# Kernel tuning notes

Hardware: AMD Instinct MI355X
Metric: run time of the kernel (lower is better)

## Reference

```python
import math
import jax, jax.numpy as jnp
import numpy as np

N, T, C = 4, 2048, 1024
H, DQK, DH = 16, 64, 4096
DV = C // H  # 64
EPS = 1e-5


def new_gelu(x):
    c = math.sqrt(2.0 / math.pi)
    return 0.5 * x * (1.0 + jnp.tanh(c * (x + 0.044715 * x ** 3)))


def layer_norm(x, w, b):
    mu = jnp.mean(x, axis=-1, keepdims=True)
    var = jnp.mean(jnp.square(x - mu), axis=-1, keepdims=True)
    return (x - mu) * jax.lax.rsqrt(var + EPS) * w + b


def setup_inputs() -> dict:
    key = jax.random.key(0)
    ks = jax.random.split(key, 8)
    def randw(k, *d):
        return jax.random.normal(k, d, dtype=jnp.float32) / math.sqrt(d[-1])
    x = jax.random.normal(ks[0], (N, T, C), dtype=jnp.float32)
    return {
        "x": x,
        "ln1_w": jnp.ones((C,), jnp.float32),
        "ln1_b": jnp.zeros((C,), jnp.float32),
        "w_q": randw(ks[1], H, DQK, C),
        "w_k": randw(ks[2], H, DQK, C),
        "w_v": randw(ks[3], H, DV, C),
        "ln2_w": jnp.ones((C,), jnp.float32),
        "ln2_b": jnp.zeros((C,), jnp.float32),
        "fc1_w": randw(ks[4], DH, C),
        "fc1_b": jnp.zeros((DH,), jnp.float32),
        "fc2_w": randw(ks[5], C, DH),
        "fc2_b": jnp.zeros((C,), jnp.float32),
    }


def attention(x, w_q, w_k, w_v):
    q = jnp.einsum('ntc,hdc->nhtd', x, w_q)
    k = jnp.einsum('ntc,hdc->nhtd', x, w_k)
    v = jnp.einsum('ntc,hdc->nhtd', x, w_v)
    a = jnp.einsum('nhtd,nhsd->nhts', q, k) / math.sqrt(DQK)
    t = jnp.arange(x.shape[1])
    causal = t[None, None, :, None] < t[None, None, None, :]  # mask future
    a = jnp.where(causal, -jnp.inf, a)
    a = jax.nn.softmax(a, axis=3)
    y = jnp.einsum('nhts,nhsd->nthd', a, v)
    return y.reshape(y.shape[0], y.shape[1], -1)


def reference(x, ln1_w, ln1_b, w_q, w_k, w_v, ln2_w, ln2_b, fc1_w, fc1_b, fc2_w, fc2_b):
    x = x + attention(layer_norm(x, ln1_w, ln1_b), w_q, w_k, w_v)
    h = layer_norm(x, ln2_w, ln2_b)
    h = new_gelu(h @ fc1_w.T + fc1_b) @ fc2_w.T + fc2_b
    return x + h
```

## Files before the change

kernel.cpp:

```cpp
#include <hip/hip_runtime.h>
#include <stdint.h>

typedef __bf16 bf16;
typedef __bf16 bf16x8 __attribute__((ext_vector_type(8)));
typedef __bf16 bf16x4 __attribute__((ext_vector_type(4)));
typedef float  f32x4  __attribute__((ext_vector_type(4)));

#define AS1 __attribute__((address_space(1)))
#define AS3 __attribute__((address_space(3)))

__device__ __forceinline__ void gload16(void* l, const void* g) {
  __builtin_amdgcn_global_load_lds((AS1 void*)(g), (AS3 void*)(l), 16, 0, 0);
}

#define NB 4
#define TT 2048
#define CC 1024
#define HH 16
#define DD 64
#define DHID 4096
#define MM (NB*TT)

__global__ __launch_bounds__(256)
void cvt_kernel(const float* __restrict__ wq, const float* __restrict__ wk,
                const float* __restrict__ wvv, const float* __restrict__ f1,
                const float* __restrict__ f2, bf16* __restrict__ dst) {
  const int NCH = 2883584;
  for (int ch = blockIdx.x*256 + threadIdx.x; ch < NCH; ch += gridDim.x*256) {
    const float* s; int base;
    if (ch < 262144)       { s = wq;  base = 0; }
    else if (ch < 524288)  { s = wk;  base = 262144; }
    else if (ch < 786432)  { s = wvv; base = 524288; }
    else if (ch < 1835008) { s = f1;  base = 786432; }
    else                   { s = f2;  base = 1835008; }
    float4 v = ((const float4*)s)[ch - base];
    bf16x4 o = { (bf16)v.x, (bf16)v.y, (bf16)v.z, (bf16)v.w };
    *(bf16x4*)(dst + (size_t)ch*4) = o;
  }
}

__global__ __launch_bounds__(256)
void ln_kernel(const float* __restrict__ x, const float* __restrict__ w,
               const float* __restrict__ b, bf16* __restrict__ out) {
  const int row = blockIdx.x;
  const int t = threadIdx.x;
  const float4 v = ((const float4*)(x + (size_t)row*CC))[t];
  float s  = v.x + v.y + v.z + v.w;
  float sq = v.x*v.x + v.y*v.y + v.z*v.z + v.w*v.w;
  #pragma unroll
  for (int m = 1; m < 64; m <<= 1) {
    s  += __shfl_xor(s, m, 64);
    sq += __shfl_xor(sq, m, 64);
  }
  __shared__ float red[8];
  const int wv = t >> 6;
  if ((t & 63) == 0) { red[wv] = s; red[4+wv] = sq; }
  __syncthreads();
  s  = red[0]+red[1]+red[2]+red[3];
  sq = red[4]+red[5]+red[6]+red[7];
  const float mu = s * (1.0f/CC);
  const float rs = rsqrtf(sq*(1.0f/CC) - mu*mu + 1e-5f);
  const float4 wv4 = ((const float4*)w)[t];
  const float4 bv4 = ((const float4*)b)[t];
  bf16x4 o = { (bf16)((v.x-mu)*rs*wv4.x + bv4.x),
               (bf16)((v.y-mu)*rs*wv4.y + bv4.y),
               (bf16)((v.z-mu)*rs*wv4.z + bv4.z),
               (bf16)((v.w-mu)*rs*wv4.w + bv4.w) };
  *(bf16x4*)(out + (size_t)row*CC + t*4) = o;
}

__device__ __forceinline__ float gelu_f(float x) {
  const float kC = 0.7978845608028654f;
  float z = kC * (x + 0.044715f * x*x*x);
  float e = __expf(2.0f*z);
  float th = 1.0f - 2.0f/(e + 1.0f);
  return 0.5f * x * (1.0f + th);
}

template<int MODE>
__global__ __launch_bounds__(256)
void gemm_kernel(const bf16* __restrict__ A, const bf16* __restrict__ B, int K,
                 void* outp, const float* __restrict__ bias, const float* resid) {
  __shared__ __align__(16) bf16 Ab[2][128*32];
  __shared__ __align__(16) bf16 Bb[2][128*32];
  const int tid  = threadIdx.x;
  const int lane = tid & 63;
  const int wv   = tid >> 6;
  const int g = lane >> 4, c = lane & 15;
  const int bm0 = blockIdx.x * 128;
  const int bn0 = blockIdx.y * 128;
  const int wm = (wv >> 1) * 64, wn = (wv & 1) * 64;

  f32x4 acc[4][4] = {};

  const int r0 = tid >> 2, c8 = tid & 3;
  const bf16* a0 = A + (size_t)(bm0 + r0)     * K + c8*8;
  const bf16* a1 = A + (size_t)(bm0 + r0 + 64)* K + c8*8;
  const bf16* b0 = B + (size_t)(bn0 + r0)     * K + c8*8;
  const bf16* b1 = B + (size_t)(bn0 + r0 + 64)* K + c8*8;

  #define GSTAGE(buf, kk)                                   \
    do {                                                    \
      gload16(&Ab[buf][wv*512],     a0 + (kk));             \
      gload16(&Ab[buf][(4+wv)*512], a1 + (kk));             \
      gload16(&Bb[buf][wv*512],     b0 + (kk));             \
      gload16(&Bb[buf][(4+wv)*512], b1 + (kk));             \
    } while (0)

  GSTAGE(0, 0);
  asm volatile("s_waitcnt vmcnt(0)" ::: "memory");
  __syncthreads();

  int cur = 0;
  for (int kt = 0; kt < K; kt += 32) {
    if (kt + 32 < K) GSTAGE(cur ^ 1, kt + 32);
    bf16x8 af[4], bfv[4];
    #pragma unroll
    for (int ms = 0; ms < 4; ++ms)
      af[ms] = *(const bf16x8*)&Ab[cur][(wm + ms*16 + c)*32 + g*8];
    #pragma unroll
    for (int ns = 0; ns < 4; ++ns)
      bfv[ns] = *(const bf16x8*)&Bb[cur][(wn + ns*16 + c)*32 + g*8];
    #pragma unroll
    for (int ms = 0; ms < 4; ++ms) {
      #pragma unroll
      for (int ns = 0; ns < 4; ++ns)
        acc[ms][ns] = __builtin_amdgcn_mfma_f32_16x16x32_bf16(af[ms], bfv[ns], acc[ms][ns], 0, 0, 0);
    }
    asm volatile("s_waitcnt vmcnt(0)" ::: "memory");
    __syncthreads();
    cur ^= 1;
  }

  #pragma unroll
  for (int ms = 0; ms < 4; ++ms) {
    const int m = bm0 + wm + ms*16 + g*4;
    #pragma unroll
    for (int ns = 0; ns < 4; ++ns) {
      const int j = bn0 + wn + ns*16 + c;
      if constexpr (MODE == 0) {
        const int which = j >> 10, hd = j & 1023;
        const int n_ = m >> 11, t_ = m & 2047;
        bf16* dst = (bf16*)outp + (size_t)which*(MM*CC)
                    + (((size_t)(n_*HH + (hd>>6))*TT + t_) << 6) + (hd & 63);
        #pragma unroll
        for (int jj = 0; jj < 4; ++jj)
          dst[(size_t)jj << 6] = (bf16)acc[ms][ns][jj];
      } else if constexpr (MODE == 1) {
        const float bb = bias[j];
        bf16* o = (bf16*)outp;
        #pragma unroll
        for (int jj = 0; jj < 4; ++jj)
          o[(size_t)(m+jj)*DHID + j] = (bf16)gelu_f(acc[ms][ns][jj] + bb);
      } else {
        const float bb = bias[j];
        float* o = (float*)outp;
        #pragma unroll
        for (int jj = 0; jj < 4; ++jj) {
          const size_t ix = (size_t)(m+jj)*CC + j;
          o[ix] = acc[ms][ns][jj] + bb + resid[ix];
        }
      }
    }
  }
  #undef GSTAGE
}

__global__ __launch_bounds__(256)
void attn_kernel(const bf16* __restrict__ qkv, const float* __restrict__ x,
                 float* __restrict__ out) {
  __shared__ __align__(16) bf16 Kb[2][64*64];
  __shared__ __align__(16) bf16 Vt[2][64*64];
  __shared__ __align__(16) bf16 Pb[4][32*64];
  const int tid = threadIdx.x, lane = tid & 63, wv = tid >> 6;
  const int g = lane >> 4, c = lane & 15;
  const int nh = blockIdx.x >> 3, pr = blockIdx.x & 7;
  const int n = nh >> 4, h = nh & 15;
  const bf16* qp = qkv + (size_t)nh * (TT*DD);
  const bf16* kp = qp + (size_t)(MM*CC);
  const bf16* vp = qp + (size_t)(2*MM*CC);
  const float INVS = 0.125f * 1.4426950408889634f;

  const int krow0 = wv*8 + (lane >> 3), kch = lane & 7;
  const int krow1 = krow0 + 32;
  const int ksw0 = ((kch ^ (krow0 & 7)) << 3);
  const int ksw1 = ((kch ^ (krow1 & 7)) << 3);
  const int vkey = tid >> 2, vqd = tid & 3;

  #define VT_WRITE(buf)                                                      \
    do {                                                                     \
      _Pragma("unroll")                                                      \
      for (int j2 = 0; j2 < 16; ++j2) {                                      \
        const int d = vqd*16 + j2;                                           \
        const int ch = ((vkey >> 3) ^ (j2 & 7) ^ (vqd << 1)) & 7;            \
        Vt[buf][d*64 + (ch << 3) + (vkey & 7)] =                             \
            (j2 < 8) ? vr0[j2] : vr1[j2 - 8];                                \
      }                                                                      \
    } while (0)

  for (int half = 0; half < 2; ++half) {
    const int qt = half ? (15 - pr) : pr;
    const int q0w = qt*128 + wv*32;
    const int ktl = (q0w + 31) >> 6;
    const int nkt = 2*qt + 2;

    bf16x8 qf[2][2];
    #pragma unroll
    for (int qs = 0; qs < 2; ++qs)
      #pragma unroll
      for (int kk = 0; kk < 2; ++kk)
        qf[qs][kk] = *(const bf16x8*)(qp + (size_t)(q0w + qs*16 + c)*DD + kk*32 + g*8);

    f32x4 o[2][4] = {};
    float mrow[2] = {-1e30f, -1e30f};
    float lrow[2] = {0.f, 0.f};

    gload16(&Kb[0][wv*512],        kp + (size_t)krow0*DD + ksw0);
    gload16(&Kb[0][2048 + wv*512], kp + (size_t)krow1*DD + ksw1);
    bf16x8 vr0 = *(const bf16x8*)(vp + (size_t)vkey*DD + vqd*16);
    bf16x8 vr1 = *(const bf16x8*)(vp + (size_t)vkey*DD + vqd*16 + 8);
    asm volatile("s_waitcnt vmcnt(0)" ::: "memory");
    VT_WRITE(0);
    __syncthreads();

    int cur = 0;
    for (int kt = 0; kt < nkt; ++kt) {
      const int nxt = cur ^ 1;
      const bool hn = (kt + 1) < nkt;
      if (hn) {
        const size_t kb = (size_t)(kt + 1) * 64;
        gload16(&Kb[nxt][wv*512],        kp + (kb + krow0)*DD + ksw0);
        gload16(&Kb[nxt][2048 + wv*512], kp + (kb + krow1)*DD + ksw1);
        vr0 = *(const bf16x8*)(vp + (kb + vkey)*DD + vqd*16);
        vr1 = *(const bf16x8*)(vp + (kb + vkey)*DD + vqd*16 + 8);
        asm volatile("" :: "v"(vr0), "v"(vr1));
      }

      if (kt <= ktl) {
        f32x4 sa[4][2] = {};
        #pragma unroll
        for (int ks = 0; ks < 4; ++ks) {
          #pragma unroll
          for (int kk = 0; kk < 2; ++kk) {
            const bf16x8 kf = *(const bf16x8*)
                &Kb[cur][(ks*16 + c)*64 + (((kk*4 + g) ^ (c & 7)) << 3)];
            #pragma unroll
            for (int qs = 0; qs < 2; ++qs)
              sa[ks][qs] = __builtin_amdgcn_mfma_f32_16x16x32_bf16(
                  kf, qf[qs][kk], sa[ks][qs], 0, 0, 0);
          }
        }
        const bool diag = (kt == ktl);
        #pragma unroll
        for (int qs = 0; qs < 2; ++qs) {
          const int q = q0w + qs*16 + c;
          float p[4][4];
          #pragma unroll
          for (int ks = 0; ks < 4; ++ks)
            #pragma unroll
            for (int jj = 0; jj < 4; ++jj) {
              float sv = sa[ks][qs][jj] * INVS;
              if (diag && (kt*64 + ks*16 + g*4 + jj > q)) sv = -1e30f;
              p[ks][jj] = sv;
            }
          float tm = p[0][0];
          #pragma unroll
          for (int ks = 0; ks < 4; ++ks)
            #pragma unroll
            for (int jj = 0; jj < 4; ++jj) tm = fmaxf(tm, p[ks][jj]);
          tm = fmaxf(tm, __shfl_xor(tm, 16, 64));
          tm = fmaxf(tm, __shfl_xor(tm, 32, 64));
          const float mo = mrow[qs];
          const float mn = fmaxf(mo, tm);
          const float sc = exp2f(mo - mn);
          mrow[qs] = mn;
          float rs = 0.f;
          #pragma unroll
          for (int ks = 0; ks < 4; ++ks)
            #pragma unroll
            for (int jj = 0; jj < 4; ++jj) {
              p[ks][jj] = exp2f(p[ks][jj] - mn);
              rs += p[ks][jj];
            }
          rs += __shfl_xor(rs, 16, 64);
          rs += __shfl_xor(rs, 32, 64);
          lrow[qs] = lrow[qs]*sc + rs;
          #pragma unroll
          for (int dt = 0; dt < 4; ++dt) o[qs][dt] *= sc;
          #pragma unroll
          for (int ks = 0; ks < 4; ++ks) {
            bf16x4 pw = { (bf16)p[ks][0], (bf16)p[ks][1],
                          (bf16)p[ks][2], (bf16)p[ks][3] };
            *(bf16x4*)&Pb[wv][(qs*16 + c)*64 +
                (((ks*2 + (g >> 1)) ^ (c & 7)) << 3) + ((g & 1) << 2)] = pw;
          }
        }
        asm volatile("s_waitcnt lgkmcnt(0)" ::: "memory");
        __builtin_amdgcn_sched_barrier(0);
        bf16x8 pbf[2][2];
        #pragma unroll
        for (int qs = 0; qs < 2; ++qs)
          #pragma unroll
          for (int kk = 0; kk < 2; ++kk)
            pbf[qs][kk] = *(const bf16x8*)
                &Pb[wv][(qs*16 + c)*64 + (((kk*4 + g) ^ (c & 7)) << 3)];
        #pragma unroll
        for (int dt = 0; dt < 4; ++dt) {
          #pragma unroll
          for (int kk = 0; kk < 2; ++kk) {
            const bf16x8 va = *(const bf16x8*)
                &Vt[cur][(dt*16 + c)*64 +
                         ((((kk*4 + g) ^ (c & 7) ^ (dt << 1)) & 7) << 3)];
            #pragma unroll
            for (int qs = 0; qs < 2; ++qs)
              o[qs][dt] = __builtin_amdgcn_mfma_f32_16x16x32_bf16(
                  va, pbf[qs][kk], o[qs][dt], 0, 0, 0);
          }
        }
      }

      asm volatile("s_waitcnt vmcnt(0)" ::: "memory");
      if (hn) VT_WRITE(nxt);
      __syncthreads();
      cur = nxt;
    }

    #pragma unroll
    for (int qs = 0; qs < 2; ++qs) {
      const float inv = 1.0f / lrow[qs];
      const int q = q0w + qs*16 + c;
      #pragma unroll
      for (int dt = 0; dt < 4; ++dt) {
        const size_t base = ((size_t)n*TT + q)*CC + h*DD + dt*16 + g*4;
        const float4 xv = *(const float4*)(x + base);
        float4 ov;
        ov.x = xv.x + o[qs][dt][0]*inv;
        ov.y = xv.y + o[qs][dt][1]*inv;
        ov.z = xv.z + o[qs][dt][2]*inv;
        ov.w = xv.w + o[qs][dt][3]*inv;
        *(float4*)(out + base) = ov;
      }
    }
  }
  #undef VT_WRITE
}

extern "C" void kernel_launch(void* const* d_in, const int* in_sizes, int n_in,
                              void* d_out, int out_size, void* d_ws, size_t ws_size,
                              hipStream_t stream) {
  const float* x    = (const float*)d_in[0];
  const float* ln1w = (const float*)d_in[1];
  const float* ln1b = (const float*)d_in[2];
  const float* wq   = (const float*)d_in[3];
  const float* wk   = (const float*)d_in[4];
  const float* wvv  = (const float*)d_in[5];
  const float* ln2w = (const float*)d_in[6];
  const float* ln2b = (const float*)d_in[7];
  const float* f1w  = (const float*)d_in[8];
  const float* f1b  = (const float*)d_in[9];
  const float* f2w  = (const float*)d_in[10];
  const float* f2b  = (const float*)d_in[11];
  float* out = (float*)d_out;

  bf16* ws     = (bf16*)d_ws;
  bf16* wfused = ws;
  bf16* wf1    = ws + 3145728;
  bf16* wf2    = ws + 7340032;
  bf16* lnb    = ws + 11534336;
  bf16* big    = ws + 19922944;
  bf16* h1     = big;

  cvt_kernel<<<2048, 256, 0, stream>>>(wq, wk, wvv, f1w, f2w, wfused);
  ln_kernel<<<MM, 256, 0, stream>>>(x, ln1w, ln1b, lnb);
  gemm_kernel<0><<<dim3(64, 24), 256, 0, stream>>>(lnb, wfused, 1024, big, nullptr, nullptr);
  attn_kernel<<<512, 256, 0, stream>>>(big, x, out);
  ln_kernel<<<MM, 256, 0, stream>>>(out, ln2w, ln2b, lnb);
  gemm_kernel<1><<<dim3(64, 32), 256, 0, stream>>>(lnb, wf1, 1024, h1, f1b, nullptr);
  gemm_kernel<2><<<dim3(64, 8), 256, 0, stream>>>(h1, wf2, 4096, out, f2b, out);
}
```

Before: 508.9 us.

## Rewrite GEMM as 8-wave 128x256 tile with staged loads and MFMA priority

Replaces the 4-wave 128x128 K=32 double-buffered GEMM with an 8-wave 128x256 tile using K=64 slices, XOR-swizzled LDS layout, and a four-phase schedule that interleaves LDS fragment reads, async global-to-LDS loads for future tiles, and MFMA bursts separated by barriers. It aims to hide global load latency, reduce LDS bank conflicts and raise MFMA utilisation. s_setprio is also added around MFMA blocks in the attention kernel. The more complex barrier and vmcnt accounting adds risk of subtle hazards, and the larger tile means fewer blocks for the small N=1024 output GEMM.

```diff
diff --git a/kernel.cpp b/kernel.cpp
--- a/kernel.cpp
+++ b/kernel.cpp
@@ -20,6 +20,10 @@
 #define DD 64
 #define DHID 4096
 #define MM (NB*TT)
+
+#define SBAR()  asm volatile("s_barrier" ::: "memory")
+#define LGKM0() do { asm volatile("s_waitcnt lgkmcnt(0)" ::: "memory"); \
+                     __builtin_amdgcn_sched_barrier(0); } while (0)
 
 __global__ __launch_bounds__(256)
 void cvt_kernel(const float* __restrict__ wq, const float* __restrict__ wk,
@@ -78,66 +82,137 @@
 }
 
 template<int MODE>
-__global__ __launch_bounds__(256)
-void gemm_kernel(const bf16* __restrict__ A, const bf16* __restrict__ B, int K,
-                 void* outp, const float* __restrict__ bias, const float* resid) {
-  __shared__ __align__(16) bf16 Ab[2][128*32];
-  __shared__ __align__(16) bf16 Bb[2][128*32];
-  const int tid  = threadIdx.x;
-  const int lane = tid & 63;
-  const int wv   = tid >> 6;
+__global__ __launch_bounds__(512, 2)
+void gemm8_kernel(const bf16* __restrict__ A, const bf16* __restrict__ B, int K,
+                  void* outp, const float* __restrict__ bias, const float* resid) {
+  __shared__ __align__(16) bf16 Ab[2][128*64];
+  __shared__ __align__(16) bf16 Bb[2][256*64];
+  const int tid = threadIdx.x, lane = tid & 63, wv = tid >> 6;
   const int g = lane >> 4, c = lane & 15;
-  const int bm0 = blockIdx.x * 128;
-  const int bn0 = blockIdx.y * 128;
-  const int wm = (wv >> 1) * 64, wn = (wv & 1) * 64;
+  const int wm = wv >> 2, wn = wv & 3;
+  const int bm0 = blockIdx.x * 128, bn0 = blockIdx.y * 256;
+  const int NT = K >> 6;
+
+  const int lr = lane >> 3;
+  const int sw8 = ((lane & 7) ^ lr) << 3;
+  const bf16* sA  = A + (size_t)(bm0 + wv*8 + lr) * K + sw8;
+  const bf16* sB0 = B + (size_t)(bn0 + wv*8 + lr) * K + sw8;
+  const bf16* sB1 = sB0 + (size_t)128 * K;
+
+  #define ST_A(b, tt)  do { \
+      gload16(&Ab[b][wv*512],         sA  + (size_t)(tt)*64); \
+      gload16(&Ab[b][4096 + wv*512],  sA  + (size_t)64*K + (size_t)(tt)*64); } while (0)
+  #define ST_B0(b, tt) do { \
+      gload16(&Bb[b][wv*512],         sB0 + (size_t)(tt)*64); \
+      gload16(&Bb[b][4096 + wv*512],  sB0 + (size_t)64*K + (size_t)(tt)*64); } while (0)
+  #define ST_B1(b, tt) do { \
+      gload16(&Bb[b][8192 + wv*512],  sB1 + (size_t)(tt)*64); \
+      gload16(&Bb[b][12288 + wv*512], sB1 + (size_t)64*K + (size_t)(tt)*64); } while (0)
+
+  ST_B0(0, 0); ST_B1(0, 0); ST_A(0, 0);
+  ST_B0(1, 1); ST_A(1, 1);
+  asm volatile("s_waitcnt vmcnt(4)" ::: "memory");
+  SBAR();
 
   f32x4 acc[4][4] = {};
-
-  const int r0 = tid >> 2, c8 = tid & 3;
-  const bf16* a0 = A + (size_t)(bm0 + r0)     * K + c8*8;
-  const bf16* a1 = A + (size_t)(bm0 + r0 + 64)* K + c8*8;
-  const bf16* b0 = B + (size_t)(bn0 + r0)     * K + c8*8;
-  const bf16* b1 = B + (size_t)(bn0 + r0 + 64)* K + c8*8;
-
-  #define GSTAGE(buf, kk)                                   \
-    do {                                                    \
-      gload16(&Ab[buf][wv*512],     a0 + (kk));             \
-      gload16(&Ab[buf][(4+wv)*512], a1 + (kk));             \
-      gload16(&Bb[buf][wv*512],     b0 + (kk));             \
-      gload16(&Bb[buf][(4+wv)*512], b1 + (kk));             \
-    } while (0)
-
-  GSTAGE(0, 0);
-  asm volatile("s_waitcnt vmcnt(0)" ::: "memory");
-  __syncthreads();
+  const int ach0 = ((0*4 + g) ^ (c & 7)) << 3;
+  const int ach1 = ((1*4 + g) ^ (c & 7)) << 3;
 
   int cur = 0;
-  for (int kt = 0; kt < K; kt += 32) {
-    if (kt + 32 < K) GSTAGE(cur ^ 1, kt + 32);
-    bf16x8 af[4], bfv[4];
-    #pragma unroll
-    for (int ms = 0; ms < 4; ++ms)
-      af[ms] = *(const bf16x8*)&Ab[cur][(wm + ms*16 + c)*32 + g*8];
-    #pragma unroll
-    for (int ns = 0; ns < 4; ++ns)
-      bfv[ns] = *(const bf16x8*)&Bb[cur][(wn + ns*16 + c)*32 + g*8];
-    #pragma unroll
-    for (int ms = 0; ms < 4; ++ms) {
-      #pragma unroll
-      for (int ns = 0; ns < 4; ++ns)
-        acc[ms][ns] = __builtin_amdgcn_mfma_f32_16x16x32_bf16(af[ms], bfv[ns], acc[ms][ns], 0, 0, 0);
-    }
-    asm volatile("s_waitcnt vmcnt(0)" ::: "memory");
-    __syncthreads();
-    cur ^= 1;
+  for (int kt = 0; kt < NT; ++kt) {
+    const int nxt = cur ^ 1;
+    const bool s1 = (kt + 1) < NT;
+    const bool s2 = (kt + 2) < NT;
+    bf16x8 af[2][2], bfv[4][2];
+
+    #pragma unroll
+    for (int m2 = 0; m2 < 2; ++m2) {
+      const int r = (wm*64 + m2*16 + c) * 64;
+      af[m2][0] = *(const bf16x8*)&Ab[cur][r + ach0];
+      af[m2][1] = *(const bf16x8*)&Ab[cur][r + ach1];
+    }
+    #pragma unroll
+    for (int n2 = 0; n2 < 2; ++n2) {
+      const int r = (wn*64 + n2*16 + c) * 64;
+      bfv[n2][0] = *(const bf16x8*)&Bb[cur][r + ach0];
+      bfv[n2][1] = *(const bf16x8*)&Bb[cur][r + ach1];
+    }
+    if (s1) ST_B1(nxt, kt + 1);
+    SBAR(); LGKM0();
+    __builtin_amdgcn_s_setprio(1);
+    #pragma unroll
+    for (int m2 = 0; m2 < 2; ++m2)
+      #pragma unroll
+      for (int n2 = 0; n2 < 2; ++n2)
+        #pragma unroll
+        for (int kk = 0; kk < 2; ++kk)
+          acc[m2][n2] = __builtin_amdgcn_mfma_f32_16x16x32_bf16(
+              af[m2][kk], bfv[n2][kk], acc[m2][n2], 0, 0, 0);
+    __builtin_amdgcn_s_setprio(0);
+    SBAR();
+
+    #pragma unroll
+    for (int n2 = 0; n2 < 2; ++n2) {
+      const int r = (wn*64 + 32 + n2*16 + c) * 64;
+      bfv[2+n2][0] = *(const bf16x8*)&Bb[cur][r + ach0];
+      bfv[2+n2][1] = *(const bf16x8*)&Bb[cur][r + ach1];
+    }
+    SBAR(); LGKM0();
+    __builtin_amdgcn_s_setprio(1);
+    #pragma unroll
+    for (int m2 = 0; m2 < 2; ++m2)
+      #pragma unroll
+      for (int n2 = 0; n2 < 2; ++n2)
+        #pragma unroll
+        for (int kk = 0; kk < 2; ++kk)
+          acc[m2][2+n2] = __builtin_amdgcn_mfma_f32_16x16x32_bf16(
+              af[m2][kk], bfv[2+n2][kk], acc[m2][2+n2], 0, 0, 0);
+    __builtin_amdgcn_s_setprio(0);
+    SBAR();
+
+    #pragma unroll
+    for (int m2 = 0; m2 < 2; ++m2) {
+      const int r = (wm*64 + 32 + m2*16 + c) * 64;
+      af[m2][0] = *(const bf16x8*)&Ab[cur][r + ach0];
+      af[m2][1] = *(const bf16x8*)&Ab[cur][r + ach1];
+    }
+    if (s2) ST_B0(cur, kt + 2);
+    SBAR(); LGKM0();
+    __builtin_amdgcn_s_setprio(1);
+    #pragma unroll
+    for (int m2 = 0; m2 < 2; ++m2)
+      #pragma unroll
+      for (int n2 = 0; n2 < 2; ++n2)
+        #pragma unroll
+        for (int kk = 0; kk < 2; ++kk)
+          acc[2+m2][n2] = __builtin_amdgcn_mfma_f32_16x16x32_bf16(
+              af[m2][kk], bfv[n2][kk], acc[2+m2][n2], 0, 0, 0);
+    __builtin_amdgcn_s_setprio(0);
+    SBAR();
+
+    if (s2) ST_A(cur, kt + 2);
+    __builtin_amdgcn_s_setprio(1);
+    #pragma unroll
+    for (int m2 = 0; m2 < 2; ++m2)
+      #pragma unroll
+      for (int n2 = 0; n2 < 2; ++n2)
+        #pragma unroll
+        for (int kk = 0; kk < 2; ++kk)
+          acc[2+m2][2+n2] = __builtin_amdgcn_mfma_f32_16x16x32_bf16(
+              af[m2][kk], bfv[2+n2][kk], acc[2+m2][2+n2], 0, 0, 0);
+    __builtin_amdgcn_s_setprio(0);
+    if (s2) asm volatile("s_waitcnt vmcnt(4)" ::: "memory");
+    else    asm volatile("s_waitcnt vmcnt(0)" ::: "memory");
+    SBAR();
+    cur = nxt;
   }
 
   #pragma unroll
   for (int ms = 0; ms < 4; ++ms) {
-    const int m = bm0 + wm + ms*16 + g*4;
+    const int m = bm0 + wm*64 + ms*16 + g*4;
     #pragma unroll
     for (int ns = 0; ns < 4; ++ns) {
-      const int j = bn0 + wn + ns*16 + c;
+      const int j = bn0 + wn*64 + ns*16 + c;
       if constexpr (MODE == 0) {
         const int which = j >> 10, hd = j & 1023;
         const int n_ = m >> 11, t_ = m & 2047;
@@ -163,7 +238,9 @@
       }
     }
   }
-  #undef GSTAGE
+  #undef ST_A
+  #undef ST_B0
+  #undef ST_B1
 }
 
 __global__ __launch_bounds__(256)
@@ -238,6 +315,7 @@
 
       if (kt <= ktl) {
         f32x4 sa[4][2] = {};
+        __builtin_amdgcn_s_setprio(1);
         #pragma unroll
         for (int ks = 0; ks < 4; ++ks) {
           #pragma unroll
@@ -250,6 +328,7 @@
                   kf, qf[qs][kk], sa[ks][qs], 0, 0, 0);
           }
         }
+        __builtin_amdgcn_s_setprio(0);
         const bool diag = (kt == ktl);
         #pragma unroll
         for (int qs = 0; qs < 2; ++qs) {
@@ -304,6 +383,7 @@
           for (int kk = 0; kk < 2; ++kk)
             pbf[qs][kk] = *(const bf16x8*)
                 &Pb[wv][(qs*16 + c)*64 + (((kk*4 + g) ^ (c & 7)) << 3)];
+        __builtin_amdgcn_s_setprio(1);
         #pragma unroll
         for (int dt = 0; dt < 4; ++dt) {
           #pragma unroll
@@ -317,6 +397,7 @@
                   va, pbf[qs][kk], o[qs][dt], 0, 0, 0);
           }
         }
+        __builtin_amdgcn_s_setprio(0);
       }
 
       asm volatile("s_waitcnt vmcnt(0)" ::: "memory");
@@ -372,9 +453,9 @@
 
   cvt_kernel<<<2048, 256, 0, stream>>>(wq, wk, wvv, f1w, f2w, wfused);
   ln_kernel<<<MM, 256, 0, stream>>>(x, ln1w, ln1b, lnb);
-  gemm_kernel<0><<<dim3(64, 24), 256, 0, stream>>>(lnb, wfused, 1024, big, nullptr, nullptr);
+  gemm8_kernel<0><<<dim3(64, 12), 512, 0, stream>>>(lnb, wfused, 1024, big, nullptr, nullptr);
   attn_kernel<<<512, 256, 0, stream>>>(big, x, out);
   ln_kernel<<<MM, 256, 0, stream>>>(out, ln2w, ln2b, lnb);
-  gemm_kernel<1><<<dim3(64, 32), 256, 0, stream>>>(lnb, wf1, 1024, h1, f1b, nullptr);
-  gemm_kernel<2><<<dim3(64, 8), 256, 0, stream>>>(h1, wf2, 4096, out, f2b, out);
-}
+  gemm8_kernel<1><<<dim3(64, 16), 512, 0, stream>>>(lnb, wf1, 1024, h1, f1b, nullptr);
+  gemm8_kernel<2><<<dim3(64, 4), 512, 0, stream>>>(h1, wf2, 4096, out, f2b, out);
+}
```

Result: slower. 530.7 us (+4.3%).
